# Optimization experiments

Hardware: AMD Instinct MI355X
Metric: run time of the kernel (lower is better)

## Reference

```python
import jax, jax.numpy as jnp
import numpy as np

HIDDEN_DIM = 128


def setup_inputs() -> dict:
    key = jax.random.key(0)
    ks = jax.random.split(key, 7)
    n_edges, edge_dim, edge_hidden, d = 20000, 16, 128, HIDDEN_DIM
    h_v = jax.random.normal(ks[0], (n_edges, d), dtype=jnp.float32)
    h_w = jax.random.normal(ks[1], (n_edges, d), dtype=jnp.float32)
    edge_features = jax.random.normal(ks[2], (n_edges, edge_dim), dtype=jnp.float32)
    W1 = jax.random.normal(ks[3], (edge_dim, edge_hidden), dtype=jnp.float32) * (1.0 / np.sqrt(edge_dim))
    b1 = jnp.zeros((edge_hidden,), dtype=jnp.float32)
    W2 = jax.random.normal(ks[4], (edge_hidden, d * d), dtype=jnp.float32) * (1.0 / np.sqrt(edge_hidden))
    b2 = jnp.zeros((d * d,), dtype=jnp.float32)
    return {"h_v": h_v, "h_w": h_w, "edge_features": edge_features,
            "W1": W1, "b1": b1, "W2": W2, "b2": b2}


def reference(h_v, h_w, edge_features, W1, b1, W2, b2):
    d = HIDDEN_DIM
    # Edge MLP: edge_dim -> edge_hidden -> d*d
    hidden = jax.nn.relu(edge_features @ W1 + b1)          # (E, edge_hidden)
    A = (hidden @ W2 + b2).reshape(-1, d, d)               # (E, d, d) per-edge matrices
    # Batched matrix-vector product: messages_e = A_e @ h_w_e
    messages = jnp.einsum('eij,ej->ei', A, h_w)            # (E, d)
    return messages
```

## Files before the change

kernel.cpp:

```cpp
#include <hip/hip_runtime.h>

#define E_EDGES 20000
#define D_DIM   128

#define NBA 132
#define NBH 313
#define NBC 320
#define NBD 250

#define SLAB_B  21504
#define BPF_SL  136

typedef _Float16 f16x8 __attribute__((ext_vector_type(8)));
typedef _Float16 f16x2 __attribute__((ext_vector_type(2)));
typedef float    floatx4 __attribute__((ext_vector_type(4)));

union F8 { f16x8 v; f16x2 h2[4]; unsigned int u[4]; };

__device__ __forceinline__ unsigned short f32_to_f16(float f) {
    _Float16 h = (_Float16)f;
    return __builtin_bit_cast(unsigned short, h);
}

__device__ __forceinline__ void gload_lds16(const void* g, void* l) {
    __builtin_amdgcn_global_load_lds(
        (const __attribute__((address_space(1))) unsigned int*)g,
        (__attribute__((address_space(3))) unsigned int*)l, 16, 0, 0);
}

__global__ __launch_bounds__(256) void prep_all(
    const float* __restrict__ W2, const float* __restrict__ b2,
    const float* __restrict__ ef, const float* __restrict__ W1,
    const float* __restrict__ b1, const float* __restrict__ hw,
    uint4* __restrict__ bpf, char* __restrict__ hslab,
    unsigned short* __restrict__ hwb, float* __restrict__ outz)
{
    __shared__ __align__(16) char pmem[34816];
    const int bx = blockIdx.x;
    const int t  = threadIdx.x;

    if (bx < NBA) {
        const int h = bx;
        if (h < 129) {
            unsigned short* tile = (unsigned short*)pmem;
            const float* src = (h < 128) ? (W2 + (size_t)h * (D_DIM * D_DIM)) : b2;
            #pragma unroll
            for (int r = 0; r < 16; ++r) {
                const float4 v = ((const float4*)src)[r * 256 + t];
                int c   = (r * 256 + t) * 4;
                int col = c >> 7;
                int k   = c & 127;
                unsigned int u0 = f32_to_f16(v.x) | ((unsigned int)f32_to_f16(v.y) << 16);
                unsigned int u1 = f32_to_f16(v.z) | ((unsigned int)f32_to_f16(v.w) << 16);
                *(uint2*)&tile[col * 136 + k] = make_uint2(u0, u1);
            }
            __syncthreads();
            #pragma unroll
            for (int r2 = 0; r2 < 8; ++r2) {
                int cidx = r2 * 256 + t;
                int ll = cidx & 63;
                int sp = (cidx >> 6) & 1;
                int gp = (cidx >> 7) & 3;
                int ks = (cidx >> 9) & 1;
                int ch = (cidx >> 10) & 1;
                int col = 64 * ch + 16 * gp + (ll & 15);
                int k0  = 64 * ks + 32 * sp + 8 * (ll >> 4);
                bpf[(size_t)h * 2048 + cidx] = *(const uint4*)&tile[col * 136 + k0];
            }
        } else {
            #pragma unroll
            for (int r2 = 0; r2 < 8; ++r2)
                bpf[(size_t)h * 2048 + r2 * 256 + t] = make_uint4(0, 0, 0, 0);
        }
    } else if (bx < NBA + NBH) {
        float* W1s = (float*)pmem;
        float* b1s = (float*)(pmem + 8192);
        float (*efs)[17] = (float(*)[17])(pmem + 8704);
        const int b  = bx - NBA;
        const int e0 = b * 64;
        #pragma unroll
        for (int i = 0; i < 2; ++i)
            *(float4*)&W1s[(i * 256 + t) * 4] = ((const float4*)W1)[i * 256 + t];
        if (t < 32) *(float4*)&b1s[t * 4] = ((const float4*)b1)[t];
        {
            int e  = t >> 2;
            int k4 = (t & 3) * 4;
            int ge = e0 + e;
            float4 v = make_float4(0.f, 0.f, 0.f, 0.f);
            if (ge < E_EDGES) v = *(const float4*)(ef + (size_t)ge * 16 + k4);
            efs[e][k4 + 0] = v.x; efs[e][k4 + 1] = v.y;
            efs[e][k4 + 2] = v.z; efs[e][k4 + 3] = v.w;
        }
        __syncthreads();
        const int e  = t & 63;
        const int hg = t >> 6;
        const int ge = e0 + e;
        const bool valid = ge < E_EDGES;
        const int eg = ge / 80;
        const int re = ge - eg * 80;
        char* slab = hslab + (size_t)eg * SLAB_B + re * 264;
        float efr[16];
        #pragma unroll
        for (int k = 0; k < 16; ++k) efr[k] = efs[e][k];
        #pragma unroll 4
        for (int hi2 = 0; hi2 < 16; ++hi2) {
            const int h0 = hg * 32 + 2 * hi2;
            float2 bb = *(const float2*)&b1s[h0];
            float a0 = bb.x, a1 = bb.y;
            #pragma unroll
            for (int k = 0; k < 16; ++k) {
                float2 wv = *(const float2*)&W1s[k * 128 + h0];
                a0 += efr[k] * wv.x;
                a1 += efr[k] * wv.y;
            }
            unsigned int pk = (unsigned int)f32_to_f16(fmaxf(a0, 0.f))
                            | ((unsigned int)f32_to_f16(fmaxf(a1, 0.f)) << 16);
            if (valid) *(unsigned int*)(slab + h0 * 2) = pk;
        }
        if (hg == 0 && valid) {
            *(unsigned int*)(slab + 128 * 2) = 0x00003C00u;
            *(unsigned int*)(slab + 130 * 2) = 0u;
        }
    } else if (bx < NBA + NBH + NBC) {
        int i0 = (bx - NBA - NBH) * 256 + t;
        for (int i = i0; i < (E_EDGES * D_DIM) / 4; i += NBC * 256) {
            const float4 v = ((const float4*)hw)[i];
            union { unsigned short u16[4]; uint2 u2; } o;
            o.u16[0] = f32_to_f16(v.x);
            o.u16[1] = f32_to_f16(v.y);
            o.u16[2] = f32_to_f16(v.z);
            o.u16[3] = f32_to_f16(v.w);
            ((uint2*)hwb)[i] = o.u2;
        }
    } else {
        int i0 = (bx - NBA - NBH - NBC) * 256 + t;
        float4* o4 = (float4*)outz;
        for (int i = i0; i < (E_EDGES * D_DIM) / 4; i += NBD * 256)
            o4[i] = make_float4(0.f, 0.f, 0.f, 0.f);
    }
}

__global__ __launch_bounds__(256, 4)
void edge_main(const uint4* __restrict__ bpf, const char* __restrict__ hslab,
               const uint4* __restrict__ hwb, float* __restrict__ out) {
    __shared__ __align__(16) char slab[SLAB_B];
    const int bx  = blockIdx.x;
    const int eg  = bx >> 2;
    const int ch  = (bx >> 1) & 1;
    const int ks  = bx & 1;
    const int tid = threadIdx.x;
    const int w   = tid >> 6;
    const int l   = tid & 63;
    const int l4  = l >> 4;
    const int lm  = l & 15;
    const int e0  = eg * 80;

    {
        const char* src = hslab + (size_t)eg * SLAB_B;
        for (int i = w; i < 21; i += 4)
            gload_lds16(src + i * 1024 + l * 16, slab + i * 1024);
    }

    F8 hwh[5][2];
    #pragma unroll
    for (int m = 0; m < 5; ++m)
        #pragma unroll
        for (int jq = 0; jq < 2; ++jq)
            hwh[m][jq].v = ((const F8*)hwb)[(e0 + 16 * m + lm) * 16 + 8 * ks + 4 * jq + l4].v;

    floatx4 C[5];
    #pragma unroll
    for (int m = 0; m < 5; ++m) C[m] = (floatx4){0.f, 0.f, 0.f, 0.f};

    __syncthreads();

    const f16x8* bpf8 = (const f16x8*)bpf;
    const int cbase = ch * 1024 + ks * 512 + w * 128 + l;

    f16x8 Bbuf[2][2];
    auto loadB = [&](int h, f16x8 (&B)[2]) {
        const f16x8* p = bpf8 + (size_t)h * 2048 + cbase;
        B[0] = p[0];
        B[1] = p[64];
    };
    auto loadHid = [&](int h4, uint2 (&hid)[5]) {
        #pragma unroll
        for (int m = 0; m < 5; ++m)
            hid[m] = *(const uint2*)(slab + (16 * m + lm) * 264 + h4 * 8);
    };
    auto group4 = [&](int h4, const uint2 (&hid)[5]) {
        #pragma unroll
        for (int hh = 0; hh < 4; ++hh) {
            const int h = 4 * h4 + hh;
            const int p = h & 1;
            f16x2 d[5];
            #pragma unroll
            for (int m = 0; m < 5; ++m) {
                unsigned int s   = (hh < 2) ? hid[m].x : hid[m].y;
                unsigned int sel = (hh & 1) ? 0x03020302u : 0x01000100u;
                d[m] = __builtin_bit_cast(f16x2, __builtin_amdgcn_perm(0u, s, sel));
            }
            #pragma unroll
            for (int m = 0; m < 5; ++m) {
                F8 a0, a1;
                #pragma unroll
                for (int i = 0; i < 4; ++i) {
                    a0.h2[i] = hwh[m][0].h2[i] * d[m];
                    a1.h2[i] = hwh[m][1].h2[i] * d[m];
                }
                C[m] = __builtin_amdgcn_mfma_f32_16x16x32_f16(a0.v, Bbuf[p][0], C[m], 0, 0, 0);
                C[m] = __builtin_amdgcn_mfma_f32_16x16x32_f16(a1.v, Bbuf[p][1], C[m], 0, 0, 0);
            }
            loadB(h + 2, Bbuf[p]);
        }
    };

    loadB(0, Bbuf[0]);
    loadB(1, Bbuf[1]);
    uint2 hidA[5], hidB[5];
    loadHid(0, hidA);
    for (int h4 = 0; h4 < 32; h4 += 2) {
        loadHid(h4 + 1, hidB);
        group4(h4, hidA);
        loadHid(h4 + 2, hidA);
        group4(h4 + 1, hidB);
    }
    group4(32, hidA);

    #pragma unroll
    for (int m = 0; m < 5; ++m)
        #pragma unroll
        for (int r = 0; r < 4; ++r)
            atomicAdd(&out[(size_t)(e0 + 16 * m + 4 * l4 + r) * D_DIM
                           + 64 * ch + 16 * w + lm], C[m][r]);
}

extern "C" void kernel_launch(void* const* d_in, const int* in_sizes, int n_in,
                              void* d_out, int out_size, void* d_ws, size_t ws_size,
                              hipStream_t stream) {
    const float* h_w = (const float*)d_in[1];
    const float* ef  = (const float*)d_in[2];
    const float* W1  = (const float*)d_in[3];
    const float* b1  = (const float*)d_in[4];
    const float* W2  = (const float*)d_in[5];
    const float* b2  = (const float*)d_in[6];
    float* out = (float*)d_out;

    char* ws = (char*)d_ws;
    uint4*          bpf   = (uint4*)ws;
    char*           hslab = ws + 4456448;
    unsigned short* hwb   = (unsigned short*)(ws + 4456448 + 5376000);

    hipLaunchKernelGGL(prep_all, dim3(NBA + NBH + NBC + NBD), dim3(256), 0, stream,
                       W2, b2, ef, W1, b1, h_w, bpf, hslab, hwb, out);
    hipLaunchKernelGGL(edge_main, dim3(1000), dim3(256), 0, stream,
                       bpf, hslab, (const uint4*)hwb, out);
}
```

Measured before the change: 180.5 us.

## Split K across waves with 4 N-tiles per wave and drop W2 repacking

The main kernel now assigns each wave a 32-wide slice of the j (k) dimension and has it compute all four 16-column output tiles per channel half, instead of splitting k across blocks. This halves the grid to 500 active blocks and reuses each scaled A fragment across four MFMAs, so fewer redundant A-scaling multiplies and fewer atomic partial sums across blocks. The W2 prep becomes a plain flat fp32-to-fp16 conversion with no LDS transpose, and the B operand is read with strided 16-byte loads straight from the row-major layout. The trade-offs are more accumulator registers (occupancy hint lowered to 2), less coalesced B loads, and each block still atomically summing across its four waves' partial k-slices.

```diff
diff --git a/kernel.cpp b/kernel.cpp
--- a/kernel.cpp
+++ b/kernel.cpp
@@ -2,14 +2,14 @@
 
 #define E_EDGES 20000
 #define D_DIM   128
-
-#define NBA 132
+#define HS      136
+
+#define NBA 544
 #define NBH 313
 #define NBC 320
 #define NBD 250
 
-#define SLAB_B  21504
-#define BPF_SL  136
+#define SLAB_B 21504
 
 typedef _Float16 f16x8 __attribute__((ext_vector_type(8)));
 typedef _Float16 f16x2 __attribute__((ext_vector_type(2)));
@@ -32,45 +32,31 @@
     const float* __restrict__ W2, const float* __restrict__ b2,
     const float* __restrict__ ef, const float* __restrict__ W1,
     const float* __restrict__ b1, const float* __restrict__ hw,
-    uint4* __restrict__ bpf, char* __restrict__ hslab,
+    unsigned short* __restrict__ w2h, char* __restrict__ hslab,
     unsigned short* __restrict__ hwb, float* __restrict__ outz)
 {
-    __shared__ __align__(16) char pmem[34816];
+    __shared__ __align__(16) char pmem[16384];
     const int bx = blockIdx.x;
     const int t  = threadIdx.x;
 
     if (bx < NBA) {
-        const int h = bx;
-        if (h < 129) {
-            unsigned short* tile = (unsigned short*)pmem;
-            const float* src = (h < 128) ? (W2 + (size_t)h * (D_DIM * D_DIM)) : b2;
-            #pragma unroll
-            for (int r = 0; r < 16; ++r) {
-                const float4 v = ((const float4*)src)[r * 256 + t];
-                int c   = (r * 256 + t) * 4;
-                int col = c >> 7;
-                int k   = c & 127;
-                unsigned int u0 = f32_to_f16(v.x) | ((unsigned int)f32_to_f16(v.y) << 16);
-                unsigned int u1 = f32_to_f16(v.z) | ((unsigned int)f32_to_f16(v.w) << 16);
-                *(uint2*)&tile[col * 136 + k] = make_uint2(u0, u1);
+        int u = bx * 256 + t;
+        #pragma unroll
+        for (int s = 0; s < 4; ++s, u += NBA * 256) {
+            int g0  = u * 4;
+            int h   = g0 >> 14;
+            int rem = g0 & 16383;
+            uint2 o = make_uint2(0u, 0u);
+            if (h < 128) {
+                float4 v = *(const float4*)(W2 + (size_t)h * 16384 + rem);
+                o.x = f32_to_f16(v.x) | ((unsigned int)f32_to_f16(v.y) << 16);
+                o.y = f32_to_f16(v.z) | ((unsigned int)f32_to_f16(v.w) << 16);
+            } else if (h == 128) {
+                float4 v = *(const float4*)(b2 + rem);
+                o.x = f32_to_f16(v.x) | ((unsigned int)f32_to_f16(v.y) << 16);
+                o.y = f32_to_f16(v.z) | ((unsigned int)f32_to_f16(v.w) << 16);
             }
-            __syncthreads();
-            #pragma unroll
-            for (int r2 = 0; r2 < 8; ++r2) {
-                int cidx = r2 * 256 + t;
-                int ll = cidx & 63;
-                int sp = (cidx >> 6) & 1;
-                int gp = (cidx >> 7) & 3;
-                int ks = (cidx >> 9) & 1;
-                int ch = (cidx >> 10) & 1;
-                int col = 64 * ch + 16 * gp + (ll & 15);
-                int k0  = 64 * ks + 32 * sp + 8 * (ll >> 4);
-                bpf[(size_t)h * 2048 + cidx] = *(const uint4*)&tile[col * 136 + k0];
-            }
-        } else {
-            #pragma unroll
-            for (int r2 = 0; r2 < 8; ++r2)
-                bpf[(size_t)h * 2048 + r2 * 256 + t] = make_uint4(0, 0, 0, 0);
+            ((uint2*)w2h)[u] = o;
         }
     } else if (bx < NBA + NBH) {
         float* W1s = (float*)pmem;
@@ -140,16 +126,16 @@
     }
 }
 
-__global__ __launch_bounds__(256, 4)
-void edge_main(const uint4* __restrict__ bpf, const char* __restrict__ hslab,
+__global__ __launch_bounds__(256, 2)
+void edge_main(const char* __restrict__ w2h, const char* __restrict__ hslab,
                const uint4* __restrict__ hwb, float* __restrict__ out) {
     __shared__ __align__(16) char slab[SLAB_B];
     const int bx  = blockIdx.x;
-    const int eg  = bx >> 2;
-    const int ch  = (bx >> 1) & 1;
-    const int ks  = bx & 1;
+    const int ch  = (bx & 7) >> 2;
+    const int eg  = (bx >> 3) * 4 + (bx & 3);
+    if (eg >= 250) return;
     const int tid = threadIdx.x;
-    const int w   = tid >> 6;
+    const int jq  = tid >> 6;
     const int l   = tid & 63;
     const int l4  = l >> 4;
     const int lm  = l & 15;
@@ -157,82 +143,76 @@
 
     {
         const char* src = hslab + (size_t)eg * SLAB_B;
-        for (int i = w; i < 21; i += 4)
+        for (int i = jq; i < 21; i += 4)
             gload_lds16(src + i * 1024 + l * 16, slab + i * 1024);
     }
 
-    F8 hwh[5][2];
+    F8 hws[5];
     #pragma unroll
     for (int m = 0; m < 5; ++m)
-        #pragma unroll
-        for (int jq = 0; jq < 2; ++jq)
-            hwh[m][jq].v = ((const F8*)hwb)[(e0 + 16 * m + lm) * 16 + 8 * ks + 4 * jq + l4].v;
-
-    floatx4 C[5];
+        hws[m].v = ((const F8*)hwb)[(e0 + 16 * m + lm) * 16 + 4 * jq + l4].v;
+
+    floatx4 C[5][4];
     #pragma unroll
-    for (int m = 0; m < 5; ++m) C[m] = (floatx4){0.f, 0.f, 0.f, 0.f};
+    for (int m = 0; m < 5; ++m)
+        #pragma unroll
+        for (int nt = 0; nt < 4; ++nt)
+            C[m][nt] = (floatx4){0.f, 0.f, 0.f, 0.f};
 
     __syncthreads();
 
-    const f16x8* bpf8 = (const f16x8*)bpf;
-    const int cbase = ch * 1024 + ks * 512 + w * 128 + l;
-
-    f16x8 Bbuf[2][2];
-    auto loadB = [&](int h, f16x8 (&B)[2]) {
-        const f16x8* p = bpf8 + (size_t)h * 2048 + cbase;
-        B[0] = p[0];
-        B[1] = p[64];
+    const char* bbase = w2h + (size_t)(((64 * ch + lm) << 7) + 32 * jq + 8 * l4) * 2;
+
+    f16x8 B[2][4];
+    auto loadB = [&](int h, f16x8 (&Bq)[4]) {
+        const char* p = bbase + (size_t)h * 32768;
+        #pragma unroll
+        for (int nt = 0; nt < 4; ++nt)
+            Bq[nt] = *(const f16x8*)(p + nt * 4096);
     };
-    auto loadHid = [&](int h4, uint2 (&hid)[5]) {
+    auto loadHid = [&](int q, uint2 (&hid)[5]) {
         #pragma unroll
         for (int m = 0; m < 5; ++m)
-            hid[m] = *(const uint2*)(slab + (16 * m + lm) * 264 + h4 * 8);
+            hid[m] = *(const uint2*)(slab + (16 * m + lm) * 264 + q * 8);
     };
-    auto group4 = [&](int h4, const uint2 (&hid)[5]) {
-        #pragma unroll
-        for (int hh = 0; hh < 4; ++hh) {
-            const int h = 4 * h4 + hh;
-            const int p = h & 1;
-            f16x2 d[5];
-            #pragma unroll
-            for (int m = 0; m < 5; ++m) {
-                unsigned int s   = (hh < 2) ? hid[m].x : hid[m].y;
-                unsigned int sel = (hh & 1) ? 0x03020302u : 0x01000100u;
-                d[m] = __builtin_bit_cast(f16x2, __builtin_amdgcn_perm(0u, s, sel));
-            }
-            #pragma unroll
-            for (int m = 0; m < 5; ++m) {
-                F8 a0, a1;
-                #pragma unroll
-                for (int i = 0; i < 4; ++i) {
-                    a0.h2[i] = hwh[m][0].h2[i] * d[m];
-                    a1.h2[i] = hwh[m][1].h2[i] * d[m];
-                }
-                C[m] = __builtin_amdgcn_mfma_f32_16x16x32_f16(a0.v, Bbuf[p][0], C[m], 0, 0, 0);
-                C[m] = __builtin_amdgcn_mfma_f32_16x16x32_f16(a1.v, Bbuf[p][1], C[m], 0, 0, 0);
-            }
-            loadB(h + 2, Bbuf[p]);
-        }
+    auto doH = [&](int h, const uint2 (&hid)[5]) {
+        const int hh = h & 3, p = h & 1;
+        #pragma unroll
+        for (int m = 0; m < 5; ++m) {
+            unsigned int s   = (hh < 2) ? hid[m].x : hid[m].y;
+            unsigned int sel = (hh & 1) ? 0x03020302u : 0x01000100u;
+            f16x2 d = __builtin_bit_cast(f16x2, __builtin_amdgcn_perm(0u, s, sel));
+            F8 a;
+            #pragma unroll
+            for (int i = 0; i < 4; ++i) a.h2[i] = hws[m].h2[i] * d;
+            #pragma unroll
+            for (int nt = 0; nt < 4; ++nt)
+                C[m][nt] = __builtin_amdgcn_mfma_f32_16x16x32_f16(a.v, B[p][nt], C[m][nt], 0, 0, 0);
+        }
+        loadB(h + 2, B[p]);
     };
 
-    loadB(0, Bbuf[0]);
-    loadB(1, Bbuf[1]);
+    loadB(0, B[0]);
+    loadB(1, B[1]);
     uint2 hidA[5], hidB[5];
     loadHid(0, hidA);
-    for (int h4 = 0; h4 < 32; h4 += 2) {
-        loadHid(h4 + 1, hidB);
-        group4(h4, hidA);
-        loadHid(h4 + 2, hidA);
-        group4(h4 + 1, hidB);
+    for (int q = 0; q < 32; q += 2) {
+        loadHid(q + 1, hidB);
+        doH(4*q + 0, hidA); doH(4*q + 1, hidA); doH(4*q + 2, hidA); doH(4*q + 3, hidA);
+        loadHid(q + 2, hidA);
+        doH(4*q + 4, hidB); doH(4*q + 5, hidB); doH(4*q + 6, hidB); doH(4*q + 7, hidB);
     }
-    group4(32, hidA);
+    doH(128, hidA); doH(129, hidA);
+    doH(130, hidA); doH(131, hidA);
 
     #pragma unroll
     for (int m = 0; m < 5; ++m)
         #pragma unroll
-        for (int r = 0; r < 4; ++r)
-            atomicAdd(&out[(size_t)(e0 + 16 * m + 4 * l4 + r) * D_DIM
-                           + 64 * ch + 16 * w + lm], C[m][r]);
+        for (int nt = 0; nt < 4; ++nt)
+            #pragma unroll
+            for (int r = 0; r < 4; ++r)
+                atomicAdd(&out[(size_t)(e0 + 16 * m + 4 * l4 + r) * D_DIM
+                               + 64 * ch + 16 * nt + lm], C[m][nt][r]);
 }
 
 extern "C" void kernel_launch(void* const* d_in, const int* in_sizes, int n_in,
@@ -247,12 +227,12 @@
     float* out = (float*)d_out;
 
     char* ws = (char*)d_ws;
-    uint4*          bpf   = (uint4*)ws;
+    unsigned short* w2h   = (unsigned short*)ws;
     char*           hslab = ws + 4456448;
     unsigned short* hwb   = (unsigned short*)(ws + 4456448 + 5376000);
 
     hipLaunchKernelGGL(prep_all, dim3(NBA + NBH + NBC + NBD), dim3(256), 0, stream,
-                       W2, b2, ef, W1, b1, h_w, bpf, hslab, hwb, out);
-    hipLaunchKernelGGL(edge_main, dim3(1000), dim3(256), 0, stream,
-                       bpf, hslab, (const uint4*)hwb, out);
-}
+                       W2, b2, ef, W1, b1, h_w, w2h, hslab, hwb, out);
+    hipLaunchKernelGGL(edge_main, dim3(504), dim3(256), 0, stream,
+                       (const char*)w2h, hslab, (const uint4*)hwb, out);
+}
```

Result: slower. 230.6 us (+27.8%).
